# Performance work log

Measured on AMD Instinct MI355X. Metric: run time of the kernel, lower is better.

## Reference

```python
import jax, jax.numpy as jnp
import numpy as np

B, C, H, W = 4, 256, 224, 224
PH, PW = 7, 7


def setup_inputs() -> dict:
    key = jax.random.key(0)
    k1, k2 = jax.random.split(key)
    x = jax.random.normal(k1, (B, C, H, W), dtype=jnp.float32)
    beta = jax.random.normal(k2, (1,), dtype=jnp.float32)
    return {"x": x, "beta": beta, "ph": PH, "pw": PW}


def reference(x, beta, ph, pw):
    Bb, Cc, Hh, Ww = x.shape
    Mh, Mw = Hh // ph, Ww // pw
    P = ph * pw            # tokens per patch (49)
    M = Mh * Mw            # number of patches
    # unfold with stride==kernel is a pure reshape/transpose:
    # (B,C,H,W) -> (B,Mh,Mw,ph,pw,C) -> (B,M,P,C); p = i*pw + j, m = mh*Mw + mw
    A = x.reshape(Bb, Cc, Mh, ph, Mw, pw).transpose(0, 2, 4, 3, 5, 1).reshape(Bb, M, P, Cc)
    # first-order similarity, softmax over last dim
    Sc = jax.nn.softmax(jnp.einsum('bmpc,bmqc->bmpq', A, A), axis=-1)   # (B,M,P,P)
    Mc = jnp.einsum('bmpq,bmqc->bmpc', Sc, A)                            # (B,M,P,C)
    # mean-centered second-order covariance (the live definition in the source)
    Ac = A - A.mean(axis=2, keepdims=True)
    Mcc = Mc - Mc.mean(axis=2, keepdims=True)
    cov = jnp.einsum('bmpc,bmqc->bmpq', Ac, Mcc) / P                     # (B,M,P,P)
    L = Sc + cov
    Ec = jnp.einsum('bmpq,bmqc->bmpc', L, A)                             # (B,M,P,C)
    # fold back: (B,M,P,C) -> (B,C,H,W)
    Ec_map = Ec.reshape(Bb, Mh, Mw, ph, pw, Cc).transpose(0, 5, 1, 3, 2, 4).reshape(Bb, Cc, Hh, Ww)
    out = x * (beta[0] * Ec_map + x)
    return out, Sc, cov, L, Ec_map
```

## Files before the change

kernel.cpp:

```cpp
#include <hip/hip_runtime.h>
#include <hip/hip_bf16.h>
#include <cstdint>
#include <cstddef>

constexpr int C_  = 256;
constexpr int H_  = 224;
constexpr int W_  = 224;
constexpr int P_  = 49;
constexpr int M_  = 1024;
constexpr int HW_ = H_ * W_;

constexpr size_t IMG_ELEMS = (size_t)4 * C_ * H_ * W_;
constexpr size_t SCO_ELEMS = (size_t)4 * M_ * P_ * P_;
constexpr size_t OFF_SC  = IMG_ELEMS;
constexpr size_t OFF_COV = OFF_SC  + SCO_ELEMS;
constexpr size_t OFF_L   = OFF_COV + SCO_ELEMS;
constexpr size_t OFF_EC  = OFF_L   + SCO_ELEMS;

typedef __attribute__((ext_vector_type(8))) short short8;
typedef __attribute__((ext_vector_type(4))) float f32x4;

constexpr size_t WS_ROW   = 56;
constexpr size_t WS_PATCH = (size_t)C_ * WS_ROW;
constexpr size_t WS_NEED  = (size_t)4096 * WS_PATCH * 2;

constexpr int SA_OFF  = 0;
constexpr int GB_OFF  = 32768;
constexpr int SCB_OFF = 39040;
constexpr int U_OFF   = 45312;
constexpr int SMEM_BYTES = 45568;


__device__ __forceinline__ int srowswz(int r) { return ((r ^ (r >> 3)) & 7) << 4; }

__device__ __forceinline__ short f2bf_s(float v) {
    __hip_bfloat16 b = __float2bfloat16(v);
    return *reinterpret_cast<short*>(&b);
}

template<bool SPLIT>
__global__ __launch_bounds__(256, 3)
void psa_kernel(const float* __restrict__ x, const float* __restrict__ betap,
                float* __restrict__ out_img, float* __restrict__ out_sc,
                float* __restrict__ out_cov, float* __restrict__ out_l,
                float* __restrict__ out_ec,
                __hip_bfloat16* __restrict__ ws_ec)
{
    __shared__ __align__(16) unsigned char smem[SMEM_BYTES];
    float* uArr = (float*)(smem + U_OFF);

    const int tid = threadIdx.x;
    const int bid = blockIdx.x;
    const int bm  = ((bid & 7) << 9) | (bid >> 3);
    const int b   = bm >> 10;
    const int m   = bm & (M_ - 1);
    const int mh  = m >> 5;
    const int mw  = m & 31;
    const float beta = betap[0];
    const size_t xpatch = (((size_t)b * C_ * H_) + (size_t)mh * 7) * W_ + (size_t)mw * 7;

    const int wid = tid >> 6, lane = tid & 63, l15 = lane & 15, lh = lane >> 4;

    {
        const int p = lane;
        const int i = p / 7, j = p - 7 * (p / 7);
        const float* xp = x + xpatch + (size_t)i * W_ + j + (size_t)(64 * wid) * HW_;
        const int swzp = srowswz(p);
        unsigned char* sbase = smem + SA_OFF + p * 512 + 128 * wid;
        #pragma unroll
        for (int g = 0; g < 8; ++g) {
            short8 pk;
            if (p < P_) {
                #pragma unroll
                for (int k = 0; k < 8; ++k)
                    pk[k] = f2bf_s(xp[(size_t)(8 * g + k) * HW_]);
            } else {
                pk = short8{0, 0, 0, 0, 0, 0, 0, 0};
            }
            *(short8*)(sbase + ((16 * g) ^ swzp)) = pk;
        }
    }
    __syncthreads();

    f32x4 gacc[4] = {f32x4{0,0,0,0}, f32x4{0,0,0,0}, f32x4{0,0,0,0}, f32x4{0,0,0,0}};
    {
        const int arow = 16 * wid + l15;
        #pragma unroll
        for (int kc = 0; kc < 8; ++kc) {
            const int cb = 64 * kc + 16 * lh;
            const short8 af = *(const short8*)(smem + SA_OFF + arow * 512 + (cb ^ srowswz(arow)));
            #pragma unroll
            for (int t = 0; t < 4; ++t) {
                const int brow = 16 * t + l15;
                const short8 bf = *(const short8*)(smem + SA_OFF + brow * 512 + (cb ^ srowswz(brow)));
                gacc[t] = __builtin_amdgcn_mfma_f32_16x16x32_bf16(af, bf, gacc[t], 0, 0, 0);
            }
        }
    }

    float mx[4];
    {
        #pragma unroll
        for (int r = 0; r < 4; ++r) {
            const int p = 16 * wid + 4 * lh + r;
            float m_ = fmaxf(fmaxf(gacc[0][r], gacc[1][r]), gacc[2][r]);
            m_ = fmaxf(m_, (l15 == 0) ? gacc[3][r] : -3.4e38f);
            float s_ = gacc[0][r] + gacc[1][r] + gacc[2][r] + ((l15 == 0) ? gacc[3][r] : 0.f);
            #pragma unroll
            for (int d = 1; d < 16; d <<= 1) {
                m_ = fmaxf(m_, __shfl_xor(m_, d));
                s_ += __shfl_xor(s_, d);
            }
            mx[r] = m_;
            if (l15 == 0 && p <= 48) uArr[p] = s_ * (1.f / 49.f);
        }
    }
    __syncthreads();

    float sc[4][4];
    {
        #pragma unroll
        for (int r = 0; r < 4; ++r) {
            const int p = 16 * wid + 4 * lh + r;
            if (p <= 48) {
                #pragma unroll
                for (int t = 0; t < 4; ++t) {
                    const int qv = 16 * t + l15;
                    const float gv = (qv <= 48) ? (gacc[t][r] - uArr[qv]) : 0.f;
                    *(__hip_bfloat16*)(smem + GB_OFF + p * 128 + ((2 * qv) ^ srowswz(p))) =
                        __float2bfloat16(gv);
                }
            }
            float e[4];
            #pragma unroll
            for (int t = 0; t < 4; ++t) {
                const int qv = 16 * t + l15;
                e[t] = (qv <= 48) ? __expf(gacc[t][r] - mx[r]) : 0.f;
            }
            float s_ = e[0] + e[1] + e[2] + e[3];
            #pragma unroll
            for (int d = 1; d < 16; d <<= 1) s_ += __shfl_xor(s_, d);
            const float rinv = 1.f / s_;
            #pragma unroll
            for (int t = 0; t < 4; ++t) sc[t][r] = e[t] * rinv;
            if (p <= 48) {
                #pragma unroll
                for (int t = 0; t < 4; ++t) {
                    const int qv = 16 * t + l15;
                    *(__hip_bfloat16*)(smem + SCB_OFF + p * 128 + ((2 * qv) ^ srowswz(p))) =
                        __float2bfloat16(sc[t][r]);
                    if (!SPLIT && qv <= 48)
                        out_sc[(size_t)bm * (P_ * P_) + p * 49 + qv] = sc[t][r];
                }
            }
        }
    }
    __syncthreads();

    f32x4 cacc[4] = {f32x4{0,0,0,0}, f32x4{0,0,0,0}, f32x4{0,0,0,0}, f32x4{0,0,0,0}};
    {
        const int arow = 16 * wid + l15;
        #pragma unroll
        for (int kc = 0; kc < 2; ++kc) {
            const int cb = 64 * kc + 16 * lh;
            const short8 af = *(const short8*)(smem + GB_OFF + arow * 128 + (cb ^ srowswz(arow)));
            #pragma unroll
            for (int t = 0; t < 4; ++t) {
                const int brow = 16 * t + l15;
                const short8 bf = *(const short8*)(smem + SCB_OFF + brow * 128 + (cb ^ srowswz(brow)));
                cacc[t] = __builtin_amdgcn_mfma_f32_16x16x32_bf16(af, bf, cacc[t], 0, 0, 0);
            }
        }
    }
    float t2[4];
    {
        #pragma unroll
        for (int r = 0; r < 4; ++r) {
            float s_ = cacc[0][r] + cacc[1][r] + cacc[2][r] + ((l15 == 0) ? cacc[3][r] : 0.f);
            #pragma unroll
            for (int d = 1; d < 16; d <<= 1) s_ += __shfl_xor(s_, d);
            t2[r] = s_ * (1.f / 49.f);
        }
    }
    __syncthreads();

    {
        #pragma unroll
        for (int t = 0; t < 4; ++t) {
            const int qv = 16 * t + l15;
            #pragma unroll
            for (int r = 0; r < 4; ++r) {
                const int p = 16 * wid + 4 * lh + r;
                if (p <= 48 && qv <= 48) {
                    const float cv = (cacc[t][r] - t2[r]) * (1.f / 49.f);
                    const float lv = sc[t][r] + cv;
                    if (!SPLIT) {
                        out_cov[(size_t)bm * (P_ * P_) + p * 49 + qv] = cv;
                        out_l  [(size_t)bm * (P_ * P_) + p * 49 + qv] = lv;
                    }
                    *(__hip_bfloat16*)(smem + GB_OFF + p * 128 + ((2 * qv) ^ srowswz(p))) =
                        __float2bfloat16(lv);
                }
            }
        }
    }
    __syncthreads();

    {
        f32x4 acc[4][4];
        #pragma unroll
        for (int i = 0; i < 4; ++i)
            #pragma unroll
            for (int j2 = 0; j2 < 4; ++j2) acc[i][j2] = f32x4{0, 0, 0, 0};

        #pragma unroll
        for (int kc = 0; kc < 2; ++kc) {
            const int cb = 64 * kc + 16 * lh;
            short8 bf[4];
            #pragma unroll
            for (int pt = 0; pt < 4; ++pt) {
                const int brow = 16 * pt + l15;
                bf[pt] = *(const short8*)(smem + GB_OFF + brow * 128 + (cb ^ srowswz(brow)));
            }
            #pragma unroll
            for (int ct = 0; ct < 4; ++ct) {
                const int c = 64 * wid + 16 * ct + l15;
                short8 af;
                #pragma unroll
                for (int j = 0; j < 8; ++j) {
                    const int q2 = 32 * kc + 8 * lh + j;
                    af[j] = *(const short*)(smem + SA_OFF + q2 * 512 + ((2 * c) ^ srowswz(q2)));
                }
                #pragma unroll
                for (int pt = 0; pt < 4; ++pt)
                    acc[ct][pt] = __builtin_amdgcn_mfma_f32_16x16x32_bf16(af, bf[pt], acc[ct][pt], 0, 0, 0);
            }
        }

        if (SPLIT) {
            __hip_bfloat16* wec = ws_ec + (size_t)bm * WS_PATCH;
            #pragma unroll
            for (int pt = 0; pt < 4; ++pt) {
                const int p = 16 * pt + l15;
                if (p >= (int)WS_ROW) continue;
                #pragma unroll
                for (int ct = 0; ct < 4; ++ct) {
                    #pragma unroll
                    for (int r = 0; r < 4; ++r) {
                        const int c = 64 * wid + 16 * ct + 4 * lh + r;
                        wec[(size_t)c * WS_ROW + p] = __float2bfloat16(acc[ct][pt][r]);
                    }
                }
            }
            float* sc_g  = out_sc  + (size_t)bm * (P_ * P_);
            float* cov_g = out_cov + (size_t)bm * (P_ * P_);
            float* l_g   = out_l   + (size_t)bm * (P_ * P_);
            for (int e = tid; e < P_ * P_; e += 256) {
                const int p = e / 49, q = e - 49 * p;
                const float scv = __bfloat162float(
                    *(const __hip_bfloat16*)(smem + SCB_OFF + p * 128 + ((2 * q) ^ srowswz(p))));
                const float lvv = __bfloat162float(
                    *(const __hip_bfloat16*)(smem + GB_OFF + p * 128 + ((2 * q) ^ srowswz(p))));
                sc_g[e]  = scv;
                l_g[e]   = lvv;
                cov_g[e] = lvv - scv;
            }
        } else {
            #pragma unroll
            for (int pt = 0; pt < 4; ++pt) {
                const int p = 16 * pt + l15;
                if (p > 48) continue;
                const int i = p / 7, j = p - 7 * (p / 7);
                const size_t base = xpatch + (size_t)i * W_ + j;
                #pragma unroll
                for (int ct = 0; ct < 4; ++ct) {
                    #pragma unroll
                    for (int r = 0; r < 4; ++r) {
                        const int c = 64 * wid + 16 * ct + 4 * lh + r;
                        const size_t g = base + (size_t)c * HW_;
                        const float ec = acc[ct][pt][r];
                        const float xv = __bfloat162float(
                            *(const __hip_bfloat16*)(smem + SA_OFF + p * 512 + ((2 * c) ^ srowswz(p))));
                        out_ec [g] = ec;
                        out_img[g] = xv * fmaf(beta, ec, xv);
                    }
                }
            }
        }
    }
}

__global__ __launch_bounds__(256)
void fold_kernel(const __hip_bfloat16* __restrict__ ws_ec,
                 const float* __restrict__ x, const float* __restrict__ betap,
                 float* __restrict__ out_img, float* __restrict__ out_ec)
{
    __shared__ __hip_bfloat16 lec[4][32][56];

    const int bid = blockIdx.x;
    const int mh  = bid & 31;
    const int bcg = bid >> 5;
    const int b   = bcg >> 6;
    const int c0  = (bcg & 63) << 2;
    const int t   = threadIdx.x;
    const float beta = betap[0];

    for (int s = t; s < 896; s += 256) {
        const int cc  = s / 224;
        const int rem = s - cc * 224;
        const int k   = rem / 7;
        const int o   = (rem - k * 7) * 8;
        const size_t base = (((size_t)(b << 10) + (mh << 5) + k) * C_ + (c0 + cc)) * WS_ROW + o;
        *(short8*)&lec[cc][k][o] = *(const short8*)&ws_ec[base];
    }
    __syncthreads();

    for (int idx = t; idx < 1568; idx += 256) {
        const int cc = idx / 392;
        const int r2 = idx - cc * 392;
        const int i  = r2 / 56;
        const int w0 = (r2 - i * 56) * 4;
        const size_t g = (((size_t)(b * C_ + c0 + cc)) * H_ + (size_t)mh * 7 + i) * W_ + w0;
        const float4 xv = *(const float4*)&x[g];
        float4 vo, ve;
        #pragma unroll
        for (int e = 0; e < 4; ++e) {
            const int w  = w0 + e;
            const int mw = w / 7;
            const int p  = i * 7 + (w - mw * 7);
            const float ec = __bfloat162float(lec[cc][mw][p]);
            const float xe = ((const float*)&xv)[e];
            ((float*)&ve)[e] = ec;
            ((float*)&vo)[e] = xe * fmaf(beta, ec, xe);
        }
        *(float4*)&out_ec [g] = ve;
        *(float4*)&out_img[g] = vo;
    }
}

extern "C" void kernel_launch(void* const* d_in, const int* in_sizes, int n_in,
                              void* d_out, int out_size, void* d_ws, size_t ws_size,
                              hipStream_t stream) {
    const float* x    = (const float*)d_in[0];
    const float* beta = (const float*)d_in[1];
    float* out = (float*)d_out;

    if (ws_size >= WS_NEED) {
        __hip_bfloat16* ws_ec = (__hip_bfloat16*)d_ws;
        psa_kernel<true><<<dim3(4 * M_), dim3(256), 0, stream>>>(
            x, beta, out, out + OFF_SC, out + OFF_COV, out + OFF_L, out + OFF_EC,
            ws_ec);
        fold_kernel<<<dim3(8192), dim3(256), 0, stream>>>(
            ws_ec, x, beta, out, out + OFF_EC);
    } else {
        psa_kernel<false><<<dim3(4 * M_), dim3(256), 0, stream>>>(
            x, beta, out, out + OFF_SC, out + OFF_COV, out + OFF_L, out + OFF_EC,
            nullptr);
    }
}
```

Baseline: 285.5 us.

## Move L·A matmul into fold kernel, pass bf16 L matrix via workspace

The first kernel no longer computes Ec. It writes only the swizzled 64x64 bf16 L matrix per patch (8 KB) to workspace, zero-padding the unused rows. A new ec_kernel reloads x strips coalesced, converts them to bf16 in LDS, recomputes Ec = L·A with MFMA, and writes out_ec and out_img. This replaces the per-patch Ec workspace (256x56 bf16) with a smaller L workspace, cutting workspace write and read traffic. In exchange it re-reads x from global memory, and the new kernel launches only 512 blocks, which may underfill the GPU.

```diff
diff --git a/kernel.cpp b/kernel.cpp
--- a/kernel.cpp
+++ b/kernel.cpp
@@ -20,22 +20,24 @@
 typedef __attribute__((ext_vector_type(8))) short short8;
 typedef __attribute__((ext_vector_type(4))) float f32x4;
 
-constexpr size_t WS_ROW   = 56;
-constexpr size_t WS_PATCH = (size_t)C_ * WS_ROW;
-constexpr size_t WS_NEED  = (size_t)4096 * WS_PATCH * 2;
+constexpr size_t WSL_PATCH = 8192;
+constexpr size_t WS_NEED   = (size_t)4096 * WSL_PATCH;
 
 constexpr int SA_OFF  = 0;
 constexpr int GB_OFF  = 32768;
-constexpr int SCB_OFF = 39040;
-constexpr int U_OFF   = 45312;
-constexpr int SMEM_BYTES = 45568;
-
+constexpr int SCB_OFF = 40960;
+constexpr int U_OFF   = 47232;
+constexpr int SMEM_BYTES = 47488;
 
 __device__ __forceinline__ int srowswz(int r) { return ((r ^ (r >> 3)) & 7) << 4; }
 
 __device__ __forceinline__ short f2bf_s(float v) {
     __hip_bfloat16 b = __float2bfloat16(v);
     return *reinterpret_cast<short*>(&b);
+}
+__device__ __forceinline__ float bf2f_s(short s) {
+    __hip_bfloat16 b = *reinterpret_cast<__hip_bfloat16*>(&s);
+    return __bfloat162float(b);
 }
 
 template<bool SPLIT>
@@ -44,7 +46,7 @@
                 float* __restrict__ out_img, float* __restrict__ out_sc,
                 float* __restrict__ out_cov, float* __restrict__ out_l,
                 float* __restrict__ out_ec,
-                __hip_bfloat16* __restrict__ ws_ec)
+                unsigned char* __restrict__ wsL)
 {
     __shared__ __align__(16) unsigned char smem[SMEM_BYTES];
     float* uArr = (float*)(smem + U_OFF);
@@ -119,6 +121,8 @@
 
     float sc[4][4];
     {
+        for (int s = tid; s < 120; s += 256)
+            *(short8*)(smem + GB_OFF + 49 * 128 + s * 16) = short8{0,0,0,0,0,0,0,0};
         #pragma unroll
         for (int r = 0; r < 4; ++r) {
             const int p = 16 * wid + 4 * lh + r;
@@ -206,13 +210,27 @@
     }
     __syncthreads();
 
-    {
+    if (SPLIT) {
+        unsigned char* dst = wsL + (size_t)bm * WSL_PATCH;
+        for (int s = tid; s < 512; s += 256)
+            *(short8*)(dst + s * 16) = *(const short8*)(smem + GB_OFF + s * 16);
+        float* sc_g  = out_sc  + (size_t)bm * (P_ * P_);
+        float* cov_g = out_cov + (size_t)bm * (P_ * P_);
+        float* l_g   = out_l   + (size_t)bm * (P_ * P_);
+        for (int e = tid; e < P_ * P_; e += 256) {
+            const int p = e / 49, q = e - 49 * p;
+            const float scv = bf2f_s(*(const short*)(smem + SCB_OFF + p * 128 + ((2 * q) ^ srowswz(p))));
+            const float lvv = bf2f_s(*(const short*)(smem + GB_OFF  + p * 128 + ((2 * q) ^ srowswz(p))));
+            sc_g[e]  = scv;
+            l_g[e]   = lvv;
+            cov_g[e] = lvv - scv;
+        }
+    } else {
         f32x4 acc[4][4];
         #pragma unroll
         for (int i = 0; i < 4; ++i)
             #pragma unroll
             for (int j2 = 0; j2 < 4; ++j2) acc[i][j2] = f32x4{0, 0, 0, 0};
-
         #pragma unroll
         for (int kc = 0; kc < 2; ++kc) {
             const int cb = 64 * kc + 16 * lh;
@@ -236,105 +254,131 @@
                     acc[ct][pt] = __builtin_amdgcn_mfma_f32_16x16x32_bf16(af, bf[pt], acc[ct][pt], 0, 0, 0);
             }
         }
-
-        if (SPLIT) {
-            __hip_bfloat16* wec = ws_ec + (size_t)bm * WS_PATCH;
-            #pragma unroll
-            for (int pt = 0; pt < 4; ++pt) {
-                const int p = 16 * pt + l15;
-                if (p >= (int)WS_ROW) continue;
-                #pragma unroll
-                for (int ct = 0; ct < 4; ++ct) {
+        #pragma unroll
+        for (int pt = 0; pt < 4; ++pt) {
+            const int p = 16 * pt + l15;
+            if (p > 48) continue;
+            const int i = p / 7, j = p - 7 * (p / 7);
+            const size_t base = xpatch + (size_t)i * W_ + j;
+            #pragma unroll
+            for (int ct = 0; ct < 4; ++ct) {
+                #pragma unroll
+                for (int r = 0; r < 4; ++r) {
+                    const int c = 64 * wid + 16 * ct + 4 * lh + r;
+                    const size_t g = base + (size_t)c * HW_;
+                    const float ec = acc[ct][pt][r];
+                    const float xv = bf2f_s(*(const short*)(smem + SA_OFF + p * 512 + ((2 * c) ^ srowswz(p))));
+                    out_ec [g] = ec;
+                    out_img[g] = xv * fmaf(beta, ec, xv);
+                }
+            }
+        }
+    }
+}
+
+__global__ __launch_bounds__(256, 2)
+void ec_kernel(const float* __restrict__ x, const float* __restrict__ betap,
+               const unsigned char* __restrict__ wsL,
+               float* __restrict__ out_img, float* __restrict__ out_ec)
+{
+    __shared__ __align__(16) unsigned char xs[8 * 4096];
+
+    const int bid   = blockIdx.x;
+    const int group = bid >> 7;
+    const int strip = bid & 127;
+    const int b  = strip >> 5, mh = strip & 31;
+    const int mw0 = group << 3;
+    const int tid = threadIdx.x;
+    const int wid = tid >> 6, lane = tid & 63, l15 = lane & 15, lh = lane >> 4;
+    const float beta = betap[0];
+
+    for (int s = tid; s < 2048; s += 256)
+        *(short8*)(xs + s * 16) = short8{0, 0, 0, 0, 0, 0, 0, 0};
+
+    short8 bfrag[2][4][2];
+    #pragma unroll
+    for (int pp = 0; pp < 2; ++pp) {
+        const int patch = 2 * wid + pp;
+        const int bm = (b << 10) + (mh << 5) + (mw0 + patch);
+        const unsigned char* Lbase = wsL + (size_t)bm * WSL_PATCH;
+        #pragma unroll
+        for (int pt = 0; pt < 4; ++pt) {
+            const int row = 16 * pt + l15;
+            #pragma unroll
+            for (int kc = 0; kc < 2; ++kc)
+                bfrag[pp][pt][kc] = *(const short8*)(Lbase + row * 128 +
+                                     ((64 * kc + 16 * lh) ^ srowswz(row)));
+        }
+    }
+    __syncthreads();
+
+    for (int ch = 0; ch < 8; ++ch) {
+        const int c0 = ch * 32;
+        for (int s = tid; s < 3136; s += 256) {
+            const int cl  = s / 98;
+            const int rem = s - cl * 98;
+            const int i   = rem / 14;
+            const int w4  = rem - i * 14;
+            const float4 v = *(const float4*)(x +
+                ((size_t)(b * C_ + c0 + cl) * H_ + (size_t)(mh * 7 + i)) * W_ +
+                mw0 * 7 + w4 * 4);
+            #pragma unroll
+            for (int e = 0; e < 4; ++e) {
+                const int w = w4 * 4 + e;
+                const int patch = w / 7, j = w - 7 * patch;
+                const int q = 7 * i + j;
+                *(short*)(xs + patch * 4096 + cl * 128 +
+                          ((2 * q) ^ srowswz(cl) ^ (patch << 4))) =
+                    f2bf_s(((const float*)&v)[e]);
+            }
+        }
+        __syncthreads();
+
+        #pragma unroll
+        for (int pp = 0; pp < 2; ++pp) {
+            const int patch = 2 * wid + pp;
+            f32x4 acc[2][4];
+            #pragma unroll
+            for (int ct = 0; ct < 2; ++ct)
+                #pragma unroll
+                for (int pt = 0; pt < 4; ++pt) acc[ct][pt] = f32x4{0, 0, 0, 0};
+            #pragma unroll
+            for (int kc = 0; kc < 2; ++kc) {
+                #pragma unroll
+                for (int ct = 0; ct < 2; ++ct) {
+                    const int cl = 16 * ct + l15;
+                    const short8 af = *(const short8*)(xs + patch * 4096 + cl * 128 +
+                        ((64 * kc + 16 * lh) ^ srowswz(cl) ^ (patch << 4)));
                     #pragma unroll
-                    for (int r = 0; r < 4; ++r) {
-                        const int c = 64 * wid + 16 * ct + 4 * lh + r;
-                        wec[(size_t)c * WS_ROW + p] = __float2bfloat16(acc[ct][pt][r]);
-                    }
-                }
-            }
-            float* sc_g  = out_sc  + (size_t)bm * (P_ * P_);
-            float* cov_g = out_cov + (size_t)bm * (P_ * P_);
-            float* l_g   = out_l   + (size_t)bm * (P_ * P_);
-            for (int e = tid; e < P_ * P_; e += 256) {
-                const int p = e / 49, q = e - 49 * p;
-                const float scv = __bfloat162float(
-                    *(const __hip_bfloat16*)(smem + SCB_OFF + p * 128 + ((2 * q) ^ srowswz(p))));
-                const float lvv = __bfloat162float(
-                    *(const __hip_bfloat16*)(smem + GB_OFF + p * 128 + ((2 * q) ^ srowswz(p))));
-                sc_g[e]  = scv;
-                l_g[e]   = lvv;
-                cov_g[e] = lvv - scv;
-            }
-        } else {
+                    for (int pt = 0; pt < 4; ++pt)
+                        acc[ct][pt] = __builtin_amdgcn_mfma_f32_16x16x32_bf16(
+                            af, bfrag[pp][pt][kc], acc[ct][pt], 0, 0, 0);
+                }
+            }
             #pragma unroll
             for (int pt = 0; pt < 4; ++pt) {
                 const int p = 16 * pt + l15;
                 if (p > 48) continue;
                 const int i = p / 7, j = p - 7 * (p / 7);
-                const size_t base = xpatch + (size_t)i * W_ + j;
-                #pragma unroll
-                for (int ct = 0; ct < 4; ++ct) {
+                #pragma unroll
+                for (int ct = 0; ct < 2; ++ct) {
                     #pragma unroll
                     for (int r = 0; r < 4; ++r) {
-                        const int c = 64 * wid + 16 * ct + 4 * lh + r;
-                        const size_t g = base + (size_t)c * HW_;
+                        const int cl = 16 * ct + 4 * lh + r;
+                        const int c  = c0 + cl;
+                        const size_t g = ((size_t)(b * C_ + c) * H_ +
+                                          (size_t)(mh * 7 + i)) * W_ +
+                                          (mw0 + patch) * 7 + j;
                         const float ec = acc[ct][pt][r];
-                        const float xv = __bfloat162float(
-                            *(const __hip_bfloat16*)(smem + SA_OFF + p * 512 + ((2 * c) ^ srowswz(p))));
+                        const float xv = bf2f_s(*(const short*)(xs + patch * 4096 +
+                            cl * 128 + ((2 * p) ^ srowswz(cl) ^ (patch << 4))));
                         out_ec [g] = ec;
                         out_img[g] = xv * fmaf(beta, ec, xv);
                     }
                 }
             }
         }
-    }
-}
-
-__global__ __launch_bounds__(256)
-void fold_kernel(const __hip_bfloat16* __restrict__ ws_ec,
-                 const float* __restrict__ x, const float* __restrict__ betap,
-                 float* __restrict__ out_img, float* __restrict__ out_ec)
-{
-    __shared__ __hip_bfloat16 lec[4][32][56];
-
-    const int bid = blockIdx.x;
-    const int mh  = bid & 31;
-    const int bcg = bid >> 5;
-    const int b   = bcg >> 6;
-    const int c0  = (bcg & 63) << 2;
-    const int t   = threadIdx.x;
-    const float beta = betap[0];
-
-    for (int s = t; s < 896; s += 256) {
-        const int cc  = s / 224;
-        const int rem = s - cc * 224;
-        const int k   = rem / 7;
-        const int o   = (rem - k * 7) * 8;
-        const size_t base = (((size_t)(b << 10) + (mh << 5) + k) * C_ + (c0 + cc)) * WS_ROW + o;
-        *(short8*)&lec[cc][k][o] = *(const short8*)&ws_ec[base];
-    }
-    __syncthreads();
-
-    for (int idx = t; idx < 1568; idx += 256) {
-        const int cc = idx / 392;
-        const int r2 = idx - cc * 392;
-        const int i  = r2 / 56;
-        const int w0 = (r2 - i * 56) * 4;
-        const size_t g = (((size_t)(b * C_ + c0 + cc)) * H_ + (size_t)mh * 7 + i) * W_ + w0;
-        const float4 xv = *(const float4*)&x[g];
-        float4 vo, ve;
-        #pragma unroll
-        for (int e = 0; e < 4; ++e) {
-            const int w  = w0 + e;
-            const int mw = w / 7;
-            const int p  = i * 7 + (w - mw * 7);
-            const float ec = __bfloat162float(lec[cc][mw][p]);
-            const float xe = ((const float*)&xv)[e];
-            ((float*)&ve)[e] = ec;
-            ((float*)&vo)[e] = xe * fmaf(beta, ec, xe);
-        }
-        *(float4*)&out_ec [g] = ve;
-        *(float4*)&out_img[g] = vo;
+        __syncthreads();
     }
 }
 
@@ -346,12 +390,12 @@
     float* out = (float*)d_out;
 
     if (ws_size >= WS_NEED) {
-        __hip_bfloat16* ws_ec = (__hip_bfloat16*)d_ws;
+        unsigned char* wsL = (unsigned char*)d_ws;
         psa_kernel<true><<<dim3(4 * M_), dim3(256), 0, stream>>>(
             x, beta, out, out + OFF_SC, out + OFF_COV, out + OFF_L, out + OFF_EC,
-            ws_ec);
-        fold_kernel<<<dim3(8192), dim3(256), 0, stream>>>(
-            ws_ec, x, beta, out, out + OFF_EC);
+            wsL);
+        ec_kernel<<<dim3(512), dim3(256), 0, stream>>>(
+            x, beta, wsL, out, out + OFF_EC);
     } else {
         psa_kernel<false><<<dim3(4 * M_), dim3(256), 0, stream>>>(
             x, beta, out, out + OFF_SC, out + OFF_COV, out + OFF_L, out + OFF_EC,
```

New measurement: 425.9 us. 1.49x slower.
